# Performance work log

Measured on AMD Instinct MI355X. Metric: run time of the kernel, lower is better.

Reference implementation:

```python
import jax, jax.numpy as jnp
import numpy as np

HIDDEN = 2048
NUM_HEADS = 32
HEAD_DIM = 64
NUM_KV = 8
GROUP = NUM_HEADS // NUM_KV
SCALE = HEAD_DIM ** -0.5
ROPE_BASE = 10000.0


def apply_rope(t):
    # t: [B, H, S, D]; standard half-split rotary embedding
    S, D = t.shape[-2], t.shape[-1]
    inv_freq = 1.0 / (ROPE_BASE ** (jnp.arange(0, D, 2, dtype=jnp.float32) / D))  # [D/2]
    ang = jnp.arange(S, dtype=jnp.float32)[:, None] * inv_freq[None, :]           # [S, D/2]
    cos, sin = jnp.cos(ang), jnp.sin(ang)
    x1, x2 = t[..., : D // 2], t[..., D // 2 :]
    return jnp.concatenate([x1 * cos - x2 * sin, x2 * cos + x1 * sin], axis=-1)


def setup_inputs() -> dict:
    key = jax.random.key(0)
    ks = jax.random.split(key, 10)
    B, S = 2, 2048
    s_in = HIDDEN ** -0.5
    s_o = (NUM_HEADS * HEAD_DIM) ** -0.5
    return {
        "x": jax.random.normal(ks[0], (B, S, HIDDEN), jnp.float32),
        "Wq": jax.random.normal(ks[1], (NUM_HEADS * HEAD_DIM, HIDDEN), jnp.float32) * s_in,
        "bq": jnp.zeros((NUM_HEADS * HEAD_DIM,), jnp.float32),
        "Wk": jax.random.normal(ks[2], (NUM_KV * HEAD_DIM, HIDDEN), jnp.float32) * s_in,
        "bk": jnp.zeros((NUM_KV * HEAD_DIM,), jnp.float32),
        "Wv": jax.random.normal(ks[3], (NUM_KV * HEAD_DIM, HIDDEN), jnp.float32) * s_in,
        "bv": jnp.zeros((NUM_KV * HEAD_DIM,), jnp.float32),
        "Wo": jax.random.normal(ks[4], (HIDDEN, NUM_HEADS * HEAD_DIM), jnp.float32) * s_o,
        "bo": jnp.zeros((HIDDEN,), jnp.float32),
        "key_weights": jax.random.normal(ks[5], (NUM_HEADS,), jnp.float32),
    }


def reference(x, Wq, bq, Wk, bk, Wv, bv, Wo, bo, key_weights):
    B, S, _ = x.shape
    q = (x @ Wq.T + bq).reshape(B, S, NUM_HEADS, HEAD_DIM).transpose(0, 2, 1, 3)
    k = (x @ Wk.T + bk).reshape(B, S, NUM_KV, HEAD_DIM).transpose(0, 2, 1, 3)
    v = (x @ Wv.T + bv).reshape(B, S, NUM_KV, HEAD_DIM).transpose(0, 2, 1, 3)
    q = apply_rope(q)
    k = apply_rope(k)
    # group queries per KV head: [B, kv, g, S, D]
    qg = q.reshape(B, NUM_KV, GROUP, S, HEAD_DIM)
    scores = jnp.einsum("bkgsd,bktd->bkgst", qg, k) * SCALE
    scores = scores * key_weights.reshape(1, NUM_KV, GROUP, 1, 1)
    causal = jnp.tril(jnp.ones((S, S), bool))
    scores = jnp.where(causal, scores, -jnp.inf)
    a = jax.nn.softmax(scores, axis=-1)
    o = jnp.einsum("bkgst,bktd->bkgsd", a, v)  # [B, kv, g, S, D]
    o = o.reshape(B, NUM_HEADS, S, HEAD_DIM).transpose(0, 2, 1, 3).reshape(B, S, NUM_HEADS * HEAD_DIM)
    return o @ Wo.T + bo
```

## Files before the change

kernel.cpp:

```cpp
#include <hip/hip_runtime.h>
#include <stdint.h>

#define S_LEN 2048
#define HID   2048
#define NH    32
#define NKV   8
#define HD    64
#define BATCH 2
#define NROWS (BATCH * S_LEN)
#define QKVN  (NH*HD + 2*NKV*HD)

typedef unsigned short u16;
typedef __bf16 bf16_t;
typedef bf16_t bf16x8 __attribute__((ext_vector_type(8)));
typedef float  f32x4  __attribute__((ext_vector_type(4)));
typedef float  f32x16 __attribute__((ext_vector_type(16)));
typedef u16    u16x8  __attribute__((ext_vector_type(8)));

#define LOG2E 1.4426950408889634f

__device__ __forceinline__ u16 f2bf(float f) {
    union { float f; uint32_t u; } v; v.f = f;
    uint32_t u = v.u;
    return (u16)((u + 0x7fffu + ((u >> 16) & 1u)) >> 16);
}

__device__ __forceinline__ unsigned cvtpk(float a, float b) {
    unsigned r;
    asm("v_cvt_pk_bf16_f32 %0, %1, %2" : "=v"(r) : "v"(a), "v"(b));
    return r;
}

__device__ __forceinline__ void plswap(unsigned &a, unsigned &b) {
    asm volatile("v_permlane32_swap_b32 %0, %1" : "+v"(a), "+v"(b));
}

__device__ __forceinline__ void llds16(const void* g, void* l) {
    __builtin_amdgcn_global_load_lds(
        (const __attribute__((address_space(1))) void*)g,
        (__attribute__((address_space(3))) void*)l,
        16, 0, 0);
}

#define LGKM0() do { asm volatile("s_waitcnt lgkmcnt(0)" ::: "memory"); \
                     __builtin_amdgcn_sched_barrier(0); } while (0)
#define BAR()   __builtin_amdgcn_s_barrier()

#define CBAR(N) do { \
    asm volatile("s_waitcnt vmcnt(" #N ")" ::: "memory"); \
    __builtin_amdgcn_s_barrier(); \
    __builtin_amdgcn_sched_barrier(0); \
} while (0)

#define CVT_GROUPS 2359296
__global__ void prep_all(const float* __restrict__ x, const float* __restrict__ wq,
                         const float* __restrict__ wk, const float* __restrict__ wv,
                         const float* __restrict__ wo,
                         const float* __restrict__ bq, const float* __restrict__ bk,
                         const float* __restrict__ bv,
                         u16* __restrict__ xb, u16* __restrict__ wqkvb, u16* __restrict__ wob,
                         float* __restrict__ rtab, float* __restrict__ bqkv) {
    int e = blockIdx.x * 256 + threadIdx.x;
    if (e < CVT_GROUPS) {
        const float* s; u16* d; int o;
        if (e < 1048576)      { s = x;  d = xb;                 o = e; }
        else if (e < 1572864) { s = wq; d = wqkvb;              o = e - 1048576; }
        else if (e < 1703936) { s = wk; d = wqkvb + 2048*2048;  o = e - 1572864; }
        else if (e < 1835008) { s = wv; d = wqkvb + 2560*2048;  o = e - 1703936; }
        else                  { s = wo; d = wob;                o = e - 1835008; }
        const float4* sp = (const float4*)s;
        float4 a = sp[2*(size_t)o], b = sp[2*(size_t)o + 1];
        u16x8 r;
        r[0]=f2bf(a.x); r[1]=f2bf(a.y); r[2]=f2bf(a.z); r[3]=f2bf(a.w);
        r[4]=f2bf(b.x); r[5]=f2bf(b.y); r[6]=f2bf(b.z); r[7]=f2bf(b.w);
        *(u16x8*)(d + 8*(size_t)o) = r;
    } else if (e < CVT_GROUPS + 65536) {
        int idx = e - CVT_GROUPS;
        int i = idx & 31, s = idx >> 5;
        float invf = exp2f(-(float)i * (13.287712379549449f / 32.0f));
        float ang = (float)s * invf;
        float sn, cs;
        sincosf(ang, &sn, &cs);
        rtab[idx] = cs;
        rtab[S_LEN*32 + idx] = sn;
    } else if (e < CVT_GROUPS + 65536 + QKVN) {
        int i = e - CVT_GROUPS - 65536;
        bqkv[i] = (i < 2048) ? bq[i] : (i < 2560 ? bk[i - 2048] : bv[i - 2560]);
    }
}


__global__ __launch_bounds__(256, 2) void gemm_qkv(
    const u16* __restrict__ A, const u16* __restrict__ Bw,
    const float* __restrict__ bias, const float* __restrict__ rtab,
    const float* __restrict__ kw,
    u16* __restrict__ qpk, u16* __restrict__ kpk, u16* __restrict__ vlin)
{
    const int M = NROWS, N = QKVN, K = HID;
    const int nbn = N >> 8;
    const int nwg = (M >> 7) * nbn;
    int wg = blockIdx.x;
    wg = (wg & 7) * (nwg >> 3) + (wg >> 3);
    const int bm = wg / nbn, bn = wg % nbn;
    const int brow = bm << 7, bcol = bn << 8;

    __shared__ u16 sbuf[3][12288];

    const int t = threadIdx.x;
    const int lane = t & 63, wid = t >> 6;
    const int wr = wid >> 1, wn = wid & 1;
    const int lr = lane & 15, lhi = lane >> 4;

    auto stageA = [&](int kt, int bi) {
        const int k0 = kt << 5;
        #pragma unroll
        for (int i = 0; i < 2; ++i) {
            const unsigned off = ((unsigned)t << 4) + ((unsigned)i << 12);
            const unsigned row = off >> 6;
            const unsigned scb = (off & 63) ^ ((row & 3) << 4);
            llds16(A + (size_t)(brow + row) * K + (k0 + (scb >> 1)), &sbuf[bi][0] + (off >> 1));
        }
        {
            const unsigned off = ((unsigned)t << 4);
            const unsigned row = off >> 6;
            const unsigned scb = (off & 63) ^ ((row & 3) << 4);
            llds16(Bw + (size_t)(bcol + row) * K + (k0 + (scb >> 1)), &sbuf[bi][4096] + (off >> 1));
        }
    };
    auto stageB = [&](int kt, int bi) {
        const int k0 = kt << 5;
        #pragma unroll
        for (int i = 1; i < 4; ++i) {
            const unsigned off = ((unsigned)t << 4) + ((unsigned)i << 12);
            const unsigned row = off >> 6;
            const unsigned scb = (off & 63) ^ ((row & 3) << 4);
            llds16(Bw + (size_t)(bcol + row) * K + (k0 + (scb >> 1)), &sbuf[bi][4096] + (off >> 1));
        }
    };

    f32x4 acc[4][8] = {};
    const int nk = K >> 5;

    stageA(0, 0); stageB(0, 0);
    stageA(1, 1); stageB(1, 1);
    asm volatile("s_waitcnt vmcnt(6)" ::: "memory");
    BAR();

    int cur = 0, st2 = 2;
    for (int kt = 0; kt < nk; ++kt) {
        const char* sA = (const char*)&sbuf[cur][0];
        const char* sB = (const char*)&sbuf[cur][4096];
        bf16x8 af[4], bfv[8];
        #pragma unroll
        for (int m = 0; m < 4; ++m) {
            const int row = wr*64 + m*16 + lr;
            af[m] = *(const bf16x8*)(sA + row*64 + ((lhi*16) ^ ((row & 3) << 4)));
        }
        #pragma unroll
        for (int n = 0; n < 4; ++n) {
            const int row = wn*128 + n*16 + lr;
            bfv[n] = *(const bf16x8*)(sB + row*64 + ((lhi*16) ^ ((row & 3) << 4)));
        }
        if (kt + 2 < nk) stageA(kt + 2, st2);
        BAR();
        LGKM0();
        __builtin_amdgcn_s_setprio(1);
        #pragma unroll
        for (int m = 0; m < 4; ++m)
            #pragma unroll
            for (int n = 0; n < 4; ++n)
                acc[m][n] = __builtin_amdgcn_mfma_f32_16x16x32_bf16(af[m], bfv[n], acc[m][n], 0, 0, 0);
        __builtin_amdgcn_s_setprio(0);
        BAR();
        #pragma unroll
        for (int n = 4; n < 8; ++n) {
            const int row = wn*128 + n*16 + lr;
            bfv[n] = *(const bf16x8*)(sB + row*64 + ((lhi*16) ^ ((row & 3) << 4)));
        }
        if (kt + 2 < nk) stageB(kt + 2, st2);
        BAR();
        LGKM0();
        __builtin_amdgcn_s_setprio(1);
        #pragma unroll
        for (int m = 0; m < 4; ++m)
            #pragma unroll
            for (int n = 4; n < 8; ++n)
                acc[m][n] = __builtin_amdgcn_mfma_f32_16x16x32_bf16(af[m], bfv[n], acc[m][n], 0, 0, 0);
        __builtin_amdgcn_s_setprio(0);
        if (kt + 2 < nk) {
            asm volatile("s_waitcnt vmcnt(6)" ::: "memory");
            BAR();
        } else if (kt + 1 < nk) {
            asm volatile("s_waitcnt vmcnt(0)" ::: "memory");
            BAR();
        }
        cur = (cur == 2) ? 0 : cur + 1;
        st2 = (st2 == 2) ? 0 : st2 + 1;
    }

    const int rowb = brow + wr*64;
    #pragma unroll
    for (int hg = 0; hg < 2; ++hg) {
        const int c64 = bcol + wn*128 + hg*64;
        const int hb  = c64 >> 6;
        if (hb < 40) {
            const bool isQ = hb < 32;
            const float sc = isQ ? (0.125f * LOG2E * kw[hb]) : 1.0f;
            u16* dst = isQ ? qpk : kpk;
            const int nheads = isQ ? 32 : 8;
            const int hloc = isQ ? hb : (hb - 32);
            #pragma unroll
            for (int m = 0; m < 4; ++m) {
                #pragma unroll
                for (int nn = 0; nn < 2; ++nn) {
                    const int n = 4*hg + nn;
                    const int i = nn*16 + lr;
                    const float b1 = bias[c64 + i];
                    const float b2 = bias[c64 + i + 32];
                    #pragma unroll
                    for (int j = 0; j < 4; ++j) {
                        const int row = rowb + m*16 + lhi*4 + j;
                        const int s = row & (S_LEN - 1);
                        const int bb = row >> 11;
                        const float x1 = acc[m][n][j] + b1;
                        const float x2 = acc[m][n+2][j] + b2;
                        const float cs = rtab[s*32 + i];
                        const float sn = rtab[S_LEN*32 + s*32 + i];
                        const size_t base = ((size_t)(bb*nheads + hloc)) * (S_LEN*64) + (size_t)s*64;
                        dst[base + i]      = f2bf((x1*cs - x2*sn) * sc);
                        dst[base + i + 32] = f2bf((x2*cs + x1*sn) * sc);
                    }
                }
            }
        } else {
            #pragma unroll
            for (int m = 0; m < 4; ++m) {
                #pragma unroll
                for (int nn = 0; nn < 4; ++nn) {
                    const int col = c64 + nn*16 + lr;
                    const float bv = bias[col];
                    #pragma unroll
                    for (int j = 0; j < 4; ++j) {
                        const int row = rowb + m*16 + lhi*4 + j;
                        vlin[(size_t)row * 512 + (col - 2560)] = f2bf(acc[m][nn + 4*hg][j] + bv);
                    }
                }
            }
        }
    }
}

__global__ __launch_bounds__(256, 2) void gemm_bt(
    const u16* __restrict__ A, const u16* __restrict__ Bw,
    const float* __restrict__ bias, float* __restrict__ C,
    int M, int N, int K)
{
    const int nbn = N >> 8;
    const int nwg = (M >> 7) * nbn;
    int wg = blockIdx.x;
    wg = (wg & 7) * (nwg >> 3) + (wg >> 3);
    const int bm = wg / nbn, bn = wg % nbn;
    const int brow = bm << 7, bcol = bn << 8;

    __shared__ u16 sbuf[3][12288];

    const int t = threadIdx.x;
    const int lane = t & 63, wid = t >> 6;
    const int wr = wid >> 1, wn = wid & 1;
    const int lr = lane & 15, lhi = lane >> 4;

    auto stageA = [&](int kt, int bi) {
        const int k0 = kt << 5;
        #pragma unroll
        for (int i = 0; i < 2; ++i) {
            const unsigned off = ((unsigned)t << 4) + ((unsigned)i << 12);
            const unsigned row = off >> 6;
            const unsigned scb = (off & 63) ^ ((row & 3) << 4);
            llds16(A + (size_t)(brow + row) * K + (k0 + (scb >> 1)), &sbuf[bi][0] + (off >> 1));
        }
        {
            const unsigned off = ((unsigned)t << 4);
            const unsigned row = off >> 6;
            const unsigned scb = (off & 63) ^ ((row & 3) << 4);
            llds16(Bw + (size_t)(bcol + row) * K + (k0 + (scb >> 1)), &sbuf[bi][4096] + (off >> 1));
        }
    };
    auto stageB = [&](int kt, int bi) {
        const int k0 = kt << 5;
        #pragma unroll
        for (int i = 1; i < 4; ++i) {
            const unsigned off = ((unsigned)t << 4) + ((unsigned)i << 12);
            const unsigned row = off >> 6;
            const unsigned scb = (off & 63) ^ ((row & 3) << 4);
            llds16(Bw + (size_t)(bcol + row) * K + (k0 + (scb >> 1)), &sbuf[bi][4096] + (off >> 1));
        }
    };

    f32x4 acc[4][8] = {};
    const int nk = K >> 5;

    stageA(0, 0); stageB(0, 0);
    stageA(1, 1); stageB(1, 1);
    asm volatile("s_waitcnt vmcnt(6)" ::: "memory");
    BAR();

    int cur = 0, st2 = 2;
    for (int kt = 0; kt < nk; ++kt) {
        const char* sA = (const char*)&sbuf[cur][0];
        const char* sB = (const char*)&sbuf[cur][4096];
        bf16x8 af[4], bfv[8];
        #pragma unroll
        for (int m = 0; m < 4; ++m) {
            const int row = wr*64 + m*16 + lr;
            af[m] = *(const bf16x8*)(sA + row*64 + ((lhi*16) ^ ((row & 3) << 4)));
        }
        #pragma unroll
        for (int n = 0; n < 4; ++n) {
            const int row = wn*128 + n*16 + lr;
            bfv[n] = *(const bf16x8*)(sB + row*64 + ((lhi*16) ^ ((row & 3) << 4)));
        }
        if (kt + 2 < nk) stageA(kt + 2, st2);
        BAR();
        LGKM0();
        __builtin_amdgcn_s_setprio(1);
        #pragma unroll
        for (int m = 0; m < 4; ++m)
            #pragma unroll
            for (int n = 0; n < 4; ++n)
                acc[m][n] = __builtin_amdgcn_mfma_f32_16x16x32_bf16(af[m], bfv[n], acc[m][n], 0, 0, 0);
        __builtin_amdgcn_s_setprio(0);
        BAR();
        #pragma unroll
        for (int n = 4; n < 8; ++n) {
            const int row = wn*128 + n*16 + lr;
            bfv[n] = *(const bf16x8*)(sB + row*64 + ((lhi*16) ^ ((row & 3) << 4)));
        }
        if (kt + 2 < nk) stageB(kt + 2, st2);
        BAR();
        LGKM0();
        __builtin_amdgcn_s_setprio(1);
        #pragma unroll
        for (int m = 0; m < 4; ++m)
            #pragma unroll
            for (int n = 4; n < 8; ++n)
                acc[m][n] = __builtin_amdgcn_mfma_f32_16x16x32_bf16(af[m], bfv[n], acc[m][n], 0, 0, 0);
        __builtin_amdgcn_s_setprio(0);
        if (kt + 2 < nk) {
            asm volatile("s_waitcnt vmcnt(6)" ::: "memory");
            BAR();
        } else if (kt + 1 < nk) {
            asm volatile("s_waitcnt vmcnt(0)" ::: "memory");
            BAR();
        }
        cur = (cur == 2) ? 0 : cur + 1;
        st2 = (st2 == 2) ? 0 : st2 + 1;
    }

    #pragma unroll
    for (int m = 0; m < 4; ++m) {
        #pragma unroll
        for (int n = 0; n < 8; ++n) {
            const int col = bcol + wn*128 + n*16 + lr;
            const float bv = bias[col];
            #pragma unroll
            for (int j = 0; j < 4; ++j) {
                const int row = brow + wr*64 + m*16 + lhi*4 + j;
                C[(size_t)row * N + col] = acc[m][n][j] + bv;
            }
        }
    }
}

__global__ void pack_vt(const u16* __restrict__ vlin, u16* __restrict__ vtb) {
    __shared__ u16 tile[64][67];
    const int st = blockIdx.x;
    const int bk = blockIdx.y;
    const int t = threadIdx.x;
    const int b = bk >> 3, kvh = bk & 7;
    const int r = t >> 2, cg = (t & 3) << 4;
    const u16* src = vlin + ((size_t)(b*S_LEN + st*64 + r)) * 512 + kvh*64 + cg;
    #pragma unroll
    for (int j = 0; j < 16; ++j) tile[r][cg + j] = src[j];
    __syncthreads();
    const int d = t >> 2, sg = (t & 3) << 4;
    u16* dst = vtb + ((size_t)(bk*64 + d)) * S_LEN + st*64 + sg;
    #pragma unroll
    for (int j = 0; j < 16; ++j) dst[j] = tile[sg + j][d];
}

__global__ __launch_bounds__(512, 4) void attn_fwd(
    const u16* __restrict__ Q,
    const u16* __restrict__ Kk,
    const u16* __restrict__ Vt,
    u16* __restrict__ O)
{
    __shared__ u16 sK[3][64 * 64];
    __shared__ u16 sV[3][64 * 64];

    const int t = threadIdx.x;
    const int lane = t & 63, wid = t >> 6;
    const int hi = lane >> 5, lq = lane & 31;
    const int bid = blockIdx.x;
    const int qb = (bid < 256) ? (7 - (bid >> 6)) : ((bid >> 6) - 4);
    const int bh = bid & 63;
    const int b = bh >> 5, h = bh & 31;
    const int kvh = h >> 2;

    const u16* Kp = Kk + ((size_t)(b*NKV + kvh)) * (S_LEN * 64);
    const u16* Vp = Vt + ((size_t)(b*NKV + kvh)) * (64 * S_LEN);

    const int q0w = qb*256 + wid*32;
    const int qg  = q0w + lq;

    const u16* Qrow = Q + (((size_t)bh) * S_LEN + qg) * 64 + 8*hi;
    bf16x8 qf[4];
    #pragma unroll
    for (int kd = 0; kd < 4; ++kd)
        qf[kd] = *(const bf16x8*)(Qrow + 16*kd);

    f32x16 accO0 = {}, accO1 = {};
    float m_run = 0.f, l_run = 0.f;

    const int ntB = 4*qb + 4;
    const int tmax_w = (q0w + 31) >> 6;

    auto stageKV = [&](int kt, int bi) {
        const int kv = kt << 6;
        const unsigned row = t >> 3, cb = (t & 7) << 4;
        const unsigned scb = cb ^ ((row & 7) << 4);
        llds16(Kp + (size_t)(kv + row) * 64 + (scb >> 1), &sK[bi][0] + t*8);
        llds16(Vp + (size_t)row * S_LEN + kv + (scb >> 1), &sV[bi][0] + t*8);
    };

    stageKV(0, 0);
    stageKV(1, 1);
    int cur = 0, st2 = 2;

    for (int tt = 0; tt < ntB; ++tt) {
        if (tt < ntB - 1) CBAR(2); else CBAR(0);
        if (tt + 2 < ntB) stageKV(tt + 2, st2);
        if (tt <= tmax_w) {
            const int kv0 = tt * 64;
            const float nm = -m_run;
            f32x16 s0, s1;
            #pragma unroll
            for (int r = 0; r < 16; ++r) { s0[r] = nm; s1[r] = nm; }
            __builtin_amdgcn_s_setprio(1);
            #pragma unroll
            for (int kd = 0; kd < 4; ++kd) {
                const unsigned bc = ((unsigned)(32*kd + 16*hi)) ^ ((lq & 7) << 4);
                bf16x8 k0 = *(const bf16x8*)((const char*)&sK[cur][0] + lq*128 + bc);
                bf16x8 k1 = *(const bf16x8*)((const char*)&sK[cur][0] + (32 + lq)*128 + bc);
                s0 = __builtin_amdgcn_mfma_f32_32x32x16_bf16(k0, qf[kd], s0, 0, 0, 0);
                s1 = __builtin_amdgcn_mfma_f32_32x32x16_bf16(k1, qf[kd], s1, 0, 0, 0);
            }
            __builtin_amdgcn_s_setprio(0);
            if (kv0 + 63 > q0w) {
                #pragma unroll
                for (int r = 0; r < 16; ++r) {
                    const int kvg = kv0 + (r & 3) + 8*(r >> 2) + 4*hi;
                    if (kvg > qg)      s0[r] = -INFINITY;
                    if (kvg + 32 > qg) s1[r] = -INFINITY;
                }
            }
            float mx[8];
            #pragma unroll
            for (int r = 0; r < 8; ++r)
                mx[r] = fmaxf(fmaxf(s0[r], s0[r+8]), fmaxf(s1[r], s1[r+8]));
            float tm = fmaxf(fmaxf(fmaxf(mx[0], mx[1]), fmaxf(mx[2], mx[3])),
                             fmaxf(fmaxf(mx[4], mx[5]), fmaxf(mx[6], mx[7])));
            tm = fmaxf(tm, __shfl_xor(tm, 32));
            if (!__all(tm <= 8.0f)) {
                const float dd = fmaxf(tm, 0.f);
                const float al = __builtin_amdgcn_exp2f(-dd);
                m_run += dd;
                l_run *= al;
                #pragma unroll
                for (int r = 0; r < 16; ++r) { accO0[r] *= al; accO1[r] *= al; }
                #pragma unroll
                for (int r = 0; r < 16; ++r) { s0[r] -= dd; s1[r] -= dd; }
            }
            #pragma unroll
            for (int r = 0; r < 16; ++r) {
                s0[r] = __builtin_amdgcn_exp2f(s0[r]);
                s1[r] = __builtin_amdgcn_exp2f(s1[r]);
            }
            float sm[8];
            #pragma unroll
            for (int r = 0; r < 8; ++r)
                sm[r] = (s0[r] + s0[r+8]) + (s1[r] + s1[r+8]);
            float rs = ((sm[0]+sm[1]) + (sm[2]+sm[3])) + ((sm[4]+sm[5]) + (sm[6]+sm[7]));
            rs += __shfl_xor(rs, 32);
            l_run += rs;

            #pragma unroll
            for (int ks = 0; ks < 4; ++ks) {
                const f32x16& e = (ks & 2) ? s1 : s0;
                const int rb = (ks & 1) * 8;
                unsigned x0 = cvtpk(e[rb + 0], e[rb + 1]);
                unsigned x1 = cvtpk(e[rb + 2], e[rb + 3]);
                unsigned y0 = cvtpk(e[rb + 4], e[rb + 5]);
                unsigned y1 = cvtpk(e[rb + 6], e[rb + 7]);
                plswap(x0, y0);
                plswap(x1, y1);
                union { unsigned u[4]; bf16x8 v; } pb;
                pb.u[0] = x0; pb.u[1] = x1; pb.u[2] = y0; pb.u[3] = y1;
                const unsigned bc = ((unsigned)(32*ks + 16*hi)) ^ ((lq & 7) << 4);
                bf16x8 v0 = *(const bf16x8*)((const char*)&sV[cur][0] + lq*128 + bc);
                bf16x8 v1 = *(const bf16x8*)((const char*)&sV[cur][0] + (32 + lq)*128 + bc);
                __builtin_amdgcn_s_setprio(1);
                accO0 = __builtin_amdgcn_mfma_f32_32x32x16_bf16(v0, pb.v, accO0, 0, 0, 0);
                accO1 = __builtin_amdgcn_mfma_f32_32x32x16_bf16(v1, pb.v, accO1, 0, 0, 0);
                __builtin_amdgcn_s_setprio(0);
            }
        }
        cur = (cur == 2) ? 0 : cur + 1;
        st2 = (st2 == 2) ? 0 : st2 + 1;
    }

    const float inv = 1.0f / l_run;
    u16* orow = O + (((size_t)(b * S_LEN) + q0w + lq)) * (NH*HD) + h*64;
    #pragma unroll
    for (int g = 0; g < 4; ++g) {
        uint2 w0, w1;
        w0.x = cvtpk(accO0[4*g + 0] * inv, accO0[4*g + 1] * inv);
        w0.y = cvtpk(accO0[4*g + 2] * inv, accO0[4*g + 3] * inv);
        *(uint2*)(orow + 8*g + 4*hi) = w0;
        w1.x = cvtpk(accO1[4*g + 0] * inv, accO1[4*g + 1] * inv);
        w1.y = cvtpk(accO1[4*g + 2] * inv, accO1[4*g + 3] * inv);
        *(uint2*)(orow + 32 + 8*g + 4*hi) = w1;
    }
}

extern "C" void kernel_launch(void* const* d_in, const int* in_sizes, int n_in,
                              void* d_out, int out_size, void* d_ws, size_t ws_size,
                              hipStream_t stream) {
    const float* x  = (const float*)d_in[0];
    const float* Wq = (const float*)d_in[1];
    const float* bq = (const float*)d_in[2];
    const float* Wk = (const float*)d_in[3];
    const float* bk = (const float*)d_in[4];
    const float* Wv = (const float*)d_in[5];
    const float* bv = (const float*)d_in[6];
    const float* Wo = (const float*)d_in[7];
    const float* bo = (const float*)d_in[8];
    const float* kw = (const float*)d_in[9];

    uint8_t* ws = (uint8_t*)d_ws;
    u16*   xb    = (u16*)(ws);
    u16*   wqkvb = (u16*)(ws + 16777216);
    u16*   wob   = (u16*)(ws + 29360128);
    u16*   qpk   = (u16*)(ws + 37748736);
    u16*   kpk   = (u16*)(ws + 54525952);
    u16*   vlin  = (u16*)(ws + 58720256);
    u16*   vtb   = (u16*)(ws + 62914560);
    u16*   ob    = (u16*)(ws + 67108864);
    float* bqkv  = (float*)(ws + 83886080);
    float* rtab  = (float*)(ws + 83898368);

    prep_all<<<9484, 256, 0, stream>>>(x, Wq, Wk, Wv, Wo, bq, bk, bv,
                                       xb, wqkvb, wob, rtab, bqkv);

    gemm_qkv<<<384, 256, 0, stream>>>(xb, wqkvb, bqkv, rtab, kw, qpk, kpk, vlin);

    pack_vt<<<dim3(32, 16), 256, 0, stream>>>(vlin, vtb);

    attn_fwd<<<dim3(512), dim3(512), 0, stream>>>(qpk, kpk, vtb, ob);

    gemm_bt<<<256, 256, 0, stream>>>(ob, wob, bo, (float*)d_out, NROWS, HID, HID);

    (void)in_sizes; (void)n_in; (void)out_size; (void)ws_size;
}
```

Baseline: 185.0 us.

## Load GEMM A operand straight to registers, staging only B through LDS

In both the QKV projection GEMM and the output GEMM, each wave now reads its A-fragment rows directly from global memory into registers, one k-step ahead. Only the B tile still goes through LDS, so shared memory per buffer shrinks and the vmcnt wait counts are retuned to the new load mix. This removes LDS writes and reads for A and frees LDS capacity. In exchange it adds per-wave global loads that are duplicated across the two column waves, strided row accesses, and more register pressure under launch_bounds(256,2).

Measured after the change: 241.7 us. 1.31x slower.

```diff
diff --git a/kernel.cpp b/kernel.cpp
--- a/kernel.cpp
+++ b/kernel.cpp
@@ -104,64 +104,53 @@
     const int bm = wg / nbn, bn = wg % nbn;
     const int brow = bm << 7, bcol = bn << 8;
 
-    __shared__ u16 sbuf[3][12288];
+    __shared__ u16 sbuf[3][8192];
 
     const int t = threadIdx.x;
     const int lane = t & 63, wid = t >> 6;
     const int wr = wid >> 1, wn = wid & 1;
     const int lr = lane & 15, lhi = lane >> 4;
 
-    auto stageA = [&](int kt, int bi) {
+    const u16* Arow = A + (size_t)(brow + wr*64 + lr) * K + lhi*8;
+
+    auto stageB4 = [&](int kt, int bi) {
         const int k0 = kt << 5;
         #pragma unroll
-        for (int i = 0; i < 2; ++i) {
+        for (int i = 0; i < 4; ++i) {
             const unsigned off = ((unsigned)t << 4) + ((unsigned)i << 12);
             const unsigned row = off >> 6;
             const unsigned scb = (off & 63) ^ ((row & 3) << 4);
-            llds16(A + (size_t)(brow + row) * K + (k0 + (scb >> 1)), &sbuf[bi][0] + (off >> 1));
-        }
-        {
-            const unsigned off = ((unsigned)t << 4);
-            const unsigned row = off >> 6;
-            const unsigned scb = (off & 63) ^ ((row & 3) << 4);
-            llds16(Bw + (size_t)(bcol + row) * K + (k0 + (scb >> 1)), &sbuf[bi][4096] + (off >> 1));
+            llds16(Bw + (size_t)(bcol + row) * K + (k0 + (scb >> 1)), &sbuf[bi][0] + (off >> 1));
         }
     };
-    auto stageB = [&](int kt, int bi) {
-        const int k0 = kt << 5;
-        #pragma unroll
-        for (int i = 1; i < 4; ++i) {
-            const unsigned off = ((unsigned)t << 4) + ((unsigned)i << 12);
-            const unsigned row = off >> 6;
-            const unsigned scb = (off & 63) ^ ((row & 3) << 4);
-            llds16(Bw + (size_t)(bcol + row) * K + (k0 + (scb >> 1)), &sbuf[bi][4096] + (off >> 1));
-        }
-    };
 
     f32x4 acc[4][8] = {};
+    bf16x8 afc[4], afn[4];
     const int nk = K >> 5;
 
-    stageA(0, 0); stageB(0, 0);
-    stageA(1, 1); stageB(1, 1);
-    asm volatile("s_waitcnt vmcnt(6)" ::: "memory");
+    #pragma unroll
+    for (int m = 0; m < 4; ++m)
+        afc[m] = *(const bf16x8*)(Arow + (size_t)(m*16) * K);
+    stageB4(0, 0);
+    stageB4(1, 1);
+    asm volatile("s_waitcnt vmcnt(4)" ::: "memory");
     BAR();
 
     int cur = 0, st2 = 2;
     for (int kt = 0; kt < nk; ++kt) {
-        const char* sA = (const char*)&sbuf[cur][0];
-        const char* sB = (const char*)&sbuf[cur][4096];
-        bf16x8 af[4], bfv[8];
-        #pragma unroll
-        for (int m = 0; m < 4; ++m) {
-            const int row = wr*64 + m*16 + lr;
-            af[m] = *(const bf16x8*)(sA + row*64 + ((lhi*16) ^ ((row & 3) << 4)));
-        }
+        const char* sB = (const char*)&sbuf[cur][0];
+        bf16x8 bfv[8];
         #pragma unroll
         for (int n = 0; n < 4; ++n) {
             const int row = wn*128 + n*16 + lr;
             bfv[n] = *(const bf16x8*)(sB + row*64 + ((lhi*16) ^ ((row & 3) << 4)));
         }
-        if (kt + 2 < nk) stageA(kt + 2, st2);
+        if (kt + 1 < nk) {
+            const int k1 = (kt + 1) << 5;
+            #pragma unroll
+            for (int m = 0; m < 4; ++m)
+                afn[m] = *(const bf16x8*)(Arow + (size_t)(m*16) * K + k1);
+        }
         BAR();
         LGKM0();
         __builtin_amdgcn_s_setprio(1);
@@ -169,7 +158,7 @@
         for (int m = 0; m < 4; ++m)
             #pragma unroll
             for (int n = 0; n < 4; ++n)
-                acc[m][n] = __builtin_amdgcn_mfma_f32_16x16x32_bf16(af[m], bfv[n], acc[m][n], 0, 0, 0);
+                acc[m][n] = __builtin_amdgcn_mfma_f32_16x16x32_bf16(afc[m], bfv[n], acc[m][n], 0, 0, 0);
         __builtin_amdgcn_s_setprio(0);
         BAR();
         #pragma unroll
@@ -177,7 +166,7 @@
             const int row = wn*128 + n*16 + lr;
             bfv[n] = *(const bf16x8*)(sB + row*64 + ((lhi*16) ^ ((row & 3) << 4)));
         }
-        if (kt + 2 < nk) stageB(kt + 2, st2);
+        if (kt + 2 < nk) stageB4(kt + 2, st2);
         BAR();
         LGKM0();
         __builtin_amdgcn_s_setprio(1);
@@ -185,15 +174,17 @@
         for (int m = 0; m < 4; ++m)
             #pragma unroll
             for (int n = 4; n < 8; ++n)
-                acc[m][n] = __builtin_amdgcn_mfma_f32_16x16x32_bf16(af[m], bfv[n], acc[m][n], 0, 0, 0);
+                acc[m][n] = __builtin_amdgcn_mfma_f32_16x16x32_bf16(afc[m], bfv[n], acc[m][n], 0, 0, 0);
         __builtin_amdgcn_s_setprio(0);
         if (kt + 2 < nk) {
-            asm volatile("s_waitcnt vmcnt(6)" ::: "memory");
+            asm volatile("s_waitcnt vmcnt(8)" ::: "memory");
             BAR();
         } else if (kt + 1 < nk) {
-            asm volatile("s_waitcnt vmcnt(0)" ::: "memory");
+            asm volatile("s_waitcnt vmcnt(4)" ::: "memory");
             BAR();
         }
+        #pragma unroll
+        for (int m = 0; m < 4; ++m) afc[m] = afn[m];
         cur = (cur == 2) ? 0 : cur + 1;
         st2 = (st2 == 2) ? 0 : st2 + 1;
     }
@@ -262,64 +253,53 @@
     const int bm = wg / nbn, bn = wg % nbn;
     const int brow = bm << 7, bcol = bn << 8;
 
-    __shared__ u16 sbuf[3][12288];
+    __shared__ u16 sbuf[3][8192];
 
     const int t = threadIdx.x;
     const int lane = t & 63, wid = t >> 6;
     const int wr = wid >> 1, wn = wid & 1;
     const int lr = lane & 15, lhi = lane >> 4;
 
-    auto stageA = [&](int kt, int bi) {
+    const u16* Arow = A + (size_t)(brow + wr*64 + lr) * K + lhi*8;
+
+    auto stageB4 = [&](int kt, int bi) {
         const int k0 = kt << 5;
         #pragma unroll
-        for (int i = 0; i < 2; ++i) {
+        for (int i = 0; i < 4; ++i) {
             const unsigned off = ((unsigned)t << 4) + ((unsigned)i << 12);
             const unsigned row = off >> 6;
             const unsigned scb = (off & 63) ^ ((row & 3) << 4);
-            llds16(A + (size_t)(brow + row) * K + (k0 + (scb >> 1)), &sbuf[bi][0] + (off >> 1));
-        }
-        {
-            const unsigned off = ((unsigned)t << 4);
-            const unsigned row = off >> 6;
-            const unsigned scb = (off & 63) ^ ((row & 3) << 4);
-            llds16(Bw + (size_t)(bcol + row) * K + (k0 + (scb >> 1)), &sbuf[bi][4096] + (off >> 1));
+            llds16(Bw + (size_t)(bcol + row) * K + (k0 + (scb >> 1)), &sbuf[bi][0] + (off >> 1));
         }
     };
-    auto stageB = [&](int kt, int bi) {
-        const int k0 = kt << 5;
-        #pragma unroll
-        for (int i = 1; i < 4; ++i) {
-            const unsigned off = ((unsigned)t << 4) + ((unsigned)i << 12);
-            const unsigned row = off >> 6;
-            const unsigned scb = (off & 63) ^ ((row & 3) << 4);
-            llds16(Bw + (size_t)(bcol + row) * K + (k0 + (scb >> 1)), &sbuf[bi][4096] + (off >> 1));
-        }
-    };
 
     f32x4 acc[4][8] = {};
+    bf16x8 afc[4], afn[4];
     const int nk = K >> 5;
 
-    stageA(0, 0); stageB(0, 0);
-    stageA(1, 1); stageB(1, 1);
-    asm volatile("s_waitcnt vmcnt(6)" ::: "memory");
+    #pragma unroll
+    for (int m = 0; m < 4; ++m)
+        afc[m] = *(const bf16x8*)(Arow + (size_t)(m*16) * K);
+    stageB4(0, 0);
+    stageB4(1, 1);
+    asm volatile("s_waitcnt vmcnt(4)" ::: "memory");
     BAR();
 
     int cur = 0, st2 = 2;
     for (int kt = 0; kt < nk; ++kt) {
-        const char* sA = (const char*)&sbuf[cur][0];
-        const char* sB = (const char*)&sbuf[cur][4096];
-        bf16x8 af[4], bfv[8];
-        #pragma unroll
-        for (int m = 0; m < 4; ++m) {
-            const int row = wr*64 + m*16 + lr;
-            af[m] = *(const bf16x8*)(sA + row*64 + ((lhi*16) ^ ((row & 3) << 4)));
-        }
+        const char* sB = (const char*)&sbuf[cur][0];
+        bf16x8 bfv[8];
         #pragma unroll
         for (int n = 0; n < 4; ++n) {
             const int row = wn*128 + n*16 + lr;
             bfv[n] = *(const bf16x8*)(sB + row*64 + ((lhi*16) ^ ((row & 3) << 4)));
         }
-        if (kt + 2 < nk) stageA(kt + 2, st2);
+        if (kt + 1 < nk) {
+            const int k1 = (kt + 1) << 5;
+            #pragma unroll
+            for (int m = 0; m < 4; ++m)
+                afn[m] = *(const bf16x8*)(Arow + (size_t)(m*16) * K + k1);
+        }
         BAR();
         LGKM0();
         __builtin_amdgcn_s_setprio(1);
@@ -327,7 +307,7 @@
         for (int m = 0; m < 4; ++m)
             #pragma unroll
             for (int n = 0; n < 4; ++n)
-                acc[m][n] = __builtin_amdgcn_mfma_f32_16x16x32_bf16(af[m], bfv[n], acc[m][n], 0, 0, 0);
+                acc[m][n] = __builtin_amdgcn_mfma_f32_16x16x32_bf16(afc[m], bfv[n], acc[m][n], 0, 0, 0);
         __builtin_amdgcn_s_setprio(0);
         BAR();
         #pragma unroll
@@ -335,7 +315,7 @@
             const int row = wn*128 + n*16 + lr;
             bfv[n] = *(const bf16x8*)(sB + row*64 + ((lhi*16) ^ ((row & 3) << 4)));
         }
-        if (kt + 2 < nk) stageB(kt + 2, st2);
+        if (kt + 2 < nk) stageB4(kt + 2, st2);
         BAR();
         LGKM0();
         __builtin_amdgcn_s_setprio(1);
@@ -343,15 +323,17 @@
         for (int m = 0; m < 4; ++m)
             #pragma unroll
             for (int n = 4; n < 8; ++n)
-                acc[m][n] = __builtin_amdgcn_mfma_f32_16x16x32_bf16(af[m], bfv[n], acc[m][n], 0, 0, 0);
+                acc[m][n] = __builtin_amdgcn_mfma_f32_16x16x32_bf16(afc[m], bfv[n], acc[m][n], 0, 0, 0);
         __builtin_amdgcn_s_setprio(0);
         if (kt + 2 < nk) {
-            asm volatile("s_waitcnt vmcnt(6)" ::: "memory");
+            asm volatile("s_waitcnt vmcnt(8)" ::: "memory");
             BAR();
         } else if (kt + 1 < nk) {
-            asm volatile("s_waitcnt vmcnt(0)" ::: "memory");
+            asm volatile("s_waitcnt vmcnt(4)" ::: "memory");
             BAR();
         }
+        #pragma unroll
+        for (int m = 0; m < 4; ++m) afc[m] = afn[m];
         cur = (cur == 2) ? 0 : cur + 1;
         st2 = (st2 == 2) ? 0 : st2 + 1;
     }
```
